# Kernel optimization log

Hardware: AMD Instinct MI355X
Metric: run time of the kernel (lower is better)

## Reference

```python
import jax, jax.numpy as jnp
import numpy as np

HID = 1024

def setup_inputs() -> dict:
    key = jax.random.key(0)
    k1, k2, k3, k4, k5 = jax.random.split(key, 5)
    B, S, H = 32, 2048, HID
    hidden = jax.random.normal(k1, (B, H), dtype=jnp.float32)
    encoder_outputs = jax.random.normal(k2, (B, S, 2 * H), dtype=jnp.float32)
    # nn.Linear(3H, H): weight (H, 3H), bias (H); nn.Linear(H, 1, bias=False): weight (1, H)
    lim_a = 1.0 / np.sqrt(3 * H)
    attn_w = jax.random.uniform(k3, (H, 3 * H), minval=-lim_a, maxval=lim_a, dtype=jnp.float32)
    attn_b = jax.random.uniform(k4, (H,), minval=-lim_a, maxval=lim_a, dtype=jnp.float32)
    lim_v = 1.0 / np.sqrt(H)
    v_w = jax.random.uniform(k5, (H,), minval=-lim_v, maxval=lim_v, dtype=jnp.float32)
    return {"hidden": hidden, "encoder_outputs": encoder_outputs,
            "attn_w": attn_w, "attn_b": attn_b, "v_w": v_w}

def reference(hidden, encoder_outputs, attn_w, attn_b, v_w):
    H = hidden.shape[-1]
    # Split attn weight: columns [:H] act on the repeated hidden, [H:] on encoder_outputs.
    # Avoids materializing the (B, S, 3H) concat; math is identical.
    w_h = attn_w[:, :H]        # (H, H)
    w_e = attn_w[:, H:]        # (H, 2H)
    hid_proj = hidden @ w_h.T + attn_b            # (B, H)
    enc_proj = jnp.einsum('bse,he->bsh', encoder_outputs, w_e)  # (B, S, H)
    energy = jnp.tanh(hid_proj[:, None, :] + enc_proj)          # (B, S, H)
    scores = jnp.einsum('bsh,h->bs', energy, v_w)               # (B, S)
    attention_weights = jax.nn.softmax(scores, axis=1)          # (B, S)
    context = jnp.einsum('bs,bse->be', attention_weights, encoder_outputs)  # (B, 2H)
    return (context, attention_weights)
```

## Files before the change

### kernel.cpp

```cpp
#include <hip/hip_runtime.h>
#include <hip/hip_bf16.h>

#define AS1 __attribute__((address_space(1)))
#define AS3 __attribute__((address_space(3)))

typedef __attribute__((ext_vector_type(4))) float  f32x4;
typedef __attribute__((ext_vector_type(8))) __bf16 bf16x8;
typedef __attribute__((ext_vector_type(2))) __bf16 bf16x2;
typedef __attribute__((ext_vector_type(4))) unsigned int uint4_;

static __device__ __forceinline__ unsigned short f2bf_rne(float f) {
    unsigned int u = __builtin_bit_cast(unsigned int, f);
    u += 0x7fffu + ((u >> 16) & 1u);
    return (unsigned short)(u >> 16);
}

static __device__ __forceinline__ unsigned int pack2(float a, float b) {
#if __has_builtin(__builtin_amdgcn_cvt_pk_bf16_f32)
    bf16x2 r = __builtin_amdgcn_cvt_pk_bf16_f32(a, b);
    return __builtin_bit_cast(unsigned int, r);
#else
    return (unsigned int)f2bf_rne(a) | ((unsigned int)f2bf_rne(b) << 16);
#endif
}

__global__ __launch_bounds__(256) void convwe_kernel(
    const float* __restrict__ attn_w, unsigned short* __restrict__ Bw)
{
    const int idx = (blockIdx.x * 256 + threadIdx.x) * 8;
    const int h = idx >> 11;
    const int e = idx & 2047;
    const float* src = attn_w + h * 3072 + 1024 + e;
    f32x4 v0 = *(const f32x4*)src;
    f32x4 v1 = *(const f32x4*)(src + 4);
    uint4_ o;
    o.x = pack2(v0.x, v0.y); o.y = pack2(v0.z, v0.w);
    o.z = pack2(v1.x, v1.y); o.w = pack2(v1.z, v1.w);
    *(uint4_*)(Bw + idx) = o;
}

__global__ __launch_bounds__(256) void convenc_kernel(
    const float* __restrict__ enc, unsigned short* __restrict__ dst)
{
    const size_t idx = ((size_t)blockIdx.x * 256 + threadIdx.x) * 8;
    f32x4 v0 = *(const f32x4*)(enc + idx);
    f32x4 v1 = *(const f32x4*)(enc + idx + 4);
    uint4_ o;
    o.x = pack2(v0.x, v0.y); o.y = pack2(v0.z, v0.w);
    o.z = pack2(v1.x, v1.y); o.w = pack2(v1.z, v1.w);
    *(uint4_*)(dst + idx) = o;
}

__global__ __launch_bounds__(256) void hidproj_kernel(
    const float* __restrict__ hidden, const float* __restrict__ attn_w,
    const float* __restrict__ attn_b, float* __restrict__ hp)
{
    __shared__ float wrow[1024];
    const int h = blockIdx.x;
    const int t = threadIdx.x;
#pragma unroll
    for (int i = 0; i < 4; ++i) wrow[t + i * 256] = attn_w[h * 3072 + t + i * 256];
    __syncthreads();
    const int wave = t >> 6, lane = t & 63;
    const float bias = attn_b[h];
    for (int b = wave; b < 32; b += 4) {
        float s = 0.f;
#pragma unroll
        for (int j = 0; j < 16; ++j)
            s = fmaf(hidden[b * 1024 + lane + j * 64], wrow[lane + j * 64], s);
#pragma unroll
        for (int off = 1; off < 64; off <<= 1) s += __shfl_xor(s, off);
        if (lane == 0) hp[b * 1024 + h] = s + bias;
    }
}

__global__ __launch_bounds__(256) void gemm_score_bf16_kernel(
    const unsigned short* __restrict__ Abf,
    const unsigned short* __restrict__ Bw,
    const float* __restrict__ hp,
    const float* __restrict__ vw,
    float* __restrict__ scores)
{
    __shared__ unsigned short As[128 * 32];
    __shared__ unsigned short Bs[128 * 32];

    const int id    = blockIdx.x;
    const int group = id >> 6;
    const int lid   = id & 63;
    const int mt    = group * 8 + (lid & 7);
    const int nt    = lid >> 3;
    const long tile_m = (long)mt * 128;
    const int  tile_n = nt * 128;

    const int t    = threadIdx.x;
    const int wave = t >> 6;
    const int lane = t & 63;
    const int quad = lane >> 4;
    const int l15  = lane & 15;

    const int ca = wave * 64 + lane;
    const int cb = (4 + wave) * 64 + lane;
    const unsigned short* apg0 = Abf + (tile_m + (ca >> 2)) * 2048 + (ca & 3) * 8;
    const unsigned short* apg1 = Abf + (tile_m + (cb >> 2)) * 2048 + (cb & 3) * 8;
    const unsigned short* bpg0 = Bw + (size_t)(tile_n + (ca >> 2)) * 2048 + (ca & 3) * 8;
    const unsigned short* bpg1 = Bw + (size_t)(tile_n + (cb >> 2)) * 2048 + (cb & 3) * 8;
    unsigned short* ald0 = &As[wave * 512];
    unsigned short* ald1 = &As[(4 + wave) * 512];
    unsigned short* bld0 = &Bs[wave * 512];
    unsigned short* bld1 = &Bs[(4 + wave) * 512];

    const int wm = (wave >> 1) * 64;
    const int wn = (wave & 1) * 64;

    int aoff[4], boff[4];
#pragma unroll
    for (int i = 0; i < 4; ++i) {
        aoff[i] = (wm + i * 16 + l15) * 32 + quad * 8;
        boff[i] = (wn + i * 16 + l15) * 32 + quad * 8;
    }

    f32x4 acc[4][4];
#pragma unroll
    for (int i = 0; i < 4; ++i)
#pragma unroll
        for (int j = 0; j < 4; ++j) acc[i][j] = (f32x4){0.f, 0.f, 0.f, 0.f};

    for (int kt = 0; kt < 64; ++kt) {
        __syncthreads();
        __builtin_amdgcn_global_load_lds((const AS1 void*)apg0, (AS3 void*)ald0, 16, 0, 0);
        __builtin_amdgcn_global_load_lds((const AS1 void*)apg1, (AS3 void*)ald1, 16, 0, 0);
        __builtin_amdgcn_global_load_lds((const AS1 void*)bpg0, (AS3 void*)bld0, 16, 0, 0);
        __builtin_amdgcn_global_load_lds((const AS1 void*)bpg1, (AS3 void*)bld1, 16, 0, 0);
        apg0 += 32; apg1 += 32; bpg0 += 32; bpg1 += 32;
        __syncthreads();

        bf16x8 af[4], bfr[4];
#pragma unroll
        for (int i = 0; i < 4; ++i) af[i]  = *(const bf16x8*)(&As[aoff[i]]);
#pragma unroll
        for (int i = 0; i < 4; ++i) bfr[i] = *(const bf16x8*)(&Bs[boff[i]]);
#pragma unroll
        for (int mi = 0; mi < 4; ++mi)
#pragma unroll
            for (int ni = 0; ni < 4; ++ni)
                acc[mi][ni] = __builtin_amdgcn_mfma_f32_16x16x32_bf16(
                    af[mi], bfr[ni], acc[mi][ni], 0, 0, 0);
    }

    const int bidx = mt >> 4;
    float vwv[4], hpv[4];
#pragma unroll
    for (int ni = 0; ni < 4; ++ni) {
        const int n = tile_n + wn + ni * 16 + l15;
        vwv[ni] = vw[n];
        hpv[ni] = hp[bidx * 1024 + n];
    }
#pragma unroll
    for (int mi = 0; mi < 4; ++mi) {
#pragma unroll
        for (int r = 0; r < 4; ++r) {
            float s = 0.f;
#pragma unroll
            for (int ni = 0; ni < 4; ++ni) {
                float x = hpv[ni] + acc[mi][ni][r];
                x = fminf(fmaxf(x, -12.f), 12.f);
                const float e  = __expf(x + x);
                const float th = (e - 1.f) * __builtin_amdgcn_rcpf(e + 1.f);
                s = fmaf(vwv[ni], th, s);
            }
            s += __shfl_xor(s, 1);
            s += __shfl_xor(s, 2);
            s += __shfl_xor(s, 4);
            s += __shfl_xor(s, 8);
            if (l15 == 0)
                atomicAdd(&scores[tile_m + wm + mi * 16 + quad * 4 + r], s);
        }
    }
}

__global__ __launch_bounds__(256) void gemm_score_kernel(
    const float* __restrict__ A, const unsigned short* __restrict__ Bw,
    const float* __restrict__ hp, const float* __restrict__ vw,
    float* __restrict__ scores)
{
    __shared__ unsigned short As[128 * 32];
    __shared__ unsigned short Bs[128 * 32];
    const int id    = blockIdx.x;
    const int group = id >> 6;
    const int lid   = id & 63;
    const int mt    = group * 8 + (lid & 7);
    const int nt    = lid >> 3;
    const long tile_m = (long)mt * 128;
    const int  tile_n = nt * 128;
    const int t = threadIdx.x, wave = t >> 6, lane = t & 63;
    const int quad = lane >> 4, l15 = lane & 15;
    const int arow = t >> 2, akc = (t & 3) * 8;
    const float* aptr0 = A + (tile_m + arow) * 2048 + akc;
    const float* aptr1 = aptr0 + 64 * 2048;
    unsigned short* ad0 = &As[t * 8];
    unsigned short* ad1 = &As[(256 + t) * 8];
    const int bc0 = wave * 128 + lane;
    const int bc1 = bc0 + 64;
    const unsigned short* bptr0 = Bw + (tile_n + (bc0 >> 2)) * 2048 + (bc0 & 3) * 8;
    const unsigned short* bptr1 = Bw + (tile_n + (bc1 >> 2)) * 2048 + (bc1 & 3) * 8;
    unsigned short* bd0 = &Bs[(wave * 2 + 0) * 512];
    unsigned short* bd1 = &Bs[(wave * 2 + 1) * 512];
    const int wm = (wave >> 1) * 64, wn = (wave & 1) * 64;
    int aoff[4], boff[4];
#pragma unroll
    for (int i = 0; i < 4; ++i) {
        aoff[i] = (wm + i * 16 + l15) * 32 + quad * 8;
        boff[i] = (wn + i * 16 + l15) * 32 + quad * 8;
    }
    f32x4 acc[4][4];
#pragma unroll
    for (int i = 0; i < 4; ++i)
#pragma unroll
        for (int j = 0; j < 4; ++j) acc[i][j] = (f32x4){0.f, 0.f, 0.f, 0.f};
    f32x4 av0 = *(const f32x4*)aptr0;
    f32x4 av1 = *(const f32x4*)(aptr0 + 4);
    f32x4 av2 = *(const f32x4*)aptr1;
    f32x4 av3 = *(const f32x4*)(aptr1 + 4);
    for (int kt = 0; kt < 64; ++kt) {
        __syncthreads();
        __builtin_amdgcn_global_load_lds((const AS1 void*)bptr0, (AS3 void*)bd0, 16, 0, 0);
        __builtin_amdgcn_global_load_lds((const AS1 void*)bptr1, (AS3 void*)bd1, 16, 0, 0);
        bptr0 += 32; bptr1 += 32;
        uint4_ w0, w1;
        w0.x = pack2(av0.x, av0.y); w0.y = pack2(av0.z, av0.w);
        w0.z = pack2(av1.x, av1.y); w0.w = pack2(av1.z, av1.w);
        w1.x = pack2(av2.x, av2.y); w1.y = pack2(av2.z, av2.w);
        w1.z = pack2(av3.x, av3.y); w1.w = pack2(av3.z, av3.w);
        *(uint4_*)ad0 = w0;
        *(uint4_*)ad1 = w1;
        if (kt < 63) {
            aptr0 += 32; aptr1 += 32;
            av0 = *(const f32x4*)aptr0;
            av1 = *(const f32x4*)(aptr0 + 4);
            av2 = *(const f32x4*)aptr1;
            av3 = *(const f32x4*)(aptr1 + 4);
        }
        __syncthreads();
        bf16x8 af[4], bfr[4];
#pragma unroll
        for (int i = 0; i < 4; ++i) af[i]  = *(const bf16x8*)(&As[aoff[i]]);
#pragma unroll
        for (int i = 0; i < 4; ++i) bfr[i] = *(const bf16x8*)(&Bs[boff[i]]);
#pragma unroll
        for (int mi = 0; mi < 4; ++mi)
#pragma unroll
            for (int ni = 0; ni < 4; ++ni)
                acc[mi][ni] = __builtin_amdgcn_mfma_f32_16x16x32_bf16(
                    af[mi], bfr[ni], acc[mi][ni], 0, 0, 0);
    }
    const int bidx = mt >> 4;
    float vwv[4], hpv[4];
#pragma unroll
    for (int ni = 0; ni < 4; ++ni) {
        const int n = tile_n + wn + ni * 16 + l15;
        vwv[ni] = vw[n];
        hpv[ni] = hp[bidx * 1024 + n];
    }
#pragma unroll
    for (int mi = 0; mi < 4; ++mi) {
#pragma unroll
        for (int r = 0; r < 4; ++r) {
            float s = 0.f;
#pragma unroll
            for (int ni = 0; ni < 4; ++ni) {
                float x = hpv[ni] + acc[mi][ni][r];
                x = fminf(fmaxf(x, -12.f), 12.f);
                const float e  = __expf(x + x);
                const float th = (e - 1.f) * __builtin_amdgcn_rcpf(e + 1.f);
                s = fmaf(vwv[ni], th, s);
            }
            s += __shfl_xor(s, 1);
            s += __shfl_xor(s, 2);
            s += __shfl_xor(s, 4);
            s += __shfl_xor(s, 8);
            if (l15 == 0)
                atomicAdd(&scores[tile_m + wm + mi * 16 + quad * 4 + r], s);
        }
    }
}

__global__ __launch_bounds__(256) void softmax_kernel(float* __restrict__ sc)
{
    __shared__ float red[8];
    const int b = blockIdx.x, t = threadIdx.x;
    const int wave = t >> 6, lane = t & 63;
    float* p = sc + b * 2048;
    float v[8];
#pragma unroll
    for (int i = 0; i < 8; ++i) v[i] = p[t + i * 256];
    float m = v[0];
#pragma unroll
    for (int i = 1; i < 8; ++i) m = fmaxf(m, v[i]);
#pragma unroll
    for (int off = 1; off < 64; off <<= 1) m = fmaxf(m, __shfl_xor(m, off));
    if (lane == 0) red[wave] = m;
    __syncthreads();
    m = fmaxf(fmaxf(red[0], red[1]), fmaxf(red[2], red[3]));
    float s = 0.f;
#pragma unroll
    for (int i = 0; i < 8; ++i) { v[i] = __expf(v[i] - m); s += v[i]; }
#pragma unroll
    for (int off = 1; off < 64; off <<= 1) s += __shfl_xor(s, off);
    if (lane == 0) red[4 + wave] = s;
    __syncthreads();
    s = red[4] + red[5] + red[6] + red[7];
    const float inv = 1.0f / s;
#pragma unroll
    for (int i = 0; i < 8; ++i) p[t + i * 256] = v[i] * inv;
}

__global__ __launch_bounds__(256) void context_part_kernel(
    const float* __restrict__ enc, const float* __restrict__ attn,
    float* __restrict__ part)
{
    const int b  = blockIdx.x >> 4;
    const int sc = blockIdx.x & 15;
    const int t  = threadIdx.x;
    const float* ep = enc + ((size_t)(b * 2048 + sc * 128)) * 2048 + t * 8;
    const float* ap = attn + b * 2048 + sc * 128;
    f32x4 a0 = (f32x4){0.f, 0.f, 0.f, 0.f};
    f32x4 a1 = (f32x4){0.f, 0.f, 0.f, 0.f};
#pragma unroll 4
    for (int s = 0; s < 128; ++s) {
        const float w = ap[s];
        f32x4 v0 = *(const f32x4*)ep;
        f32x4 v1 = *(const f32x4*)(ep + 4);
        a0 += w * v0;
        a1 += w * v1;
        ep += 2048;
    }
    float* pp = part + ((size_t)(b * 16 + sc)) * 2048 + t * 8;
    *(f32x4*)pp = a0;
    *(f32x4*)(pp + 4) = a1;
}

__global__ __launch_bounds__(256) void context_reduce_kernel(
    const float* __restrict__ part, float* __restrict__ ctx)
{
    const int idx = blockIdx.x * 256 + threadIdx.x;
    const int b = idx >> 11, e = idx & 2047;
    const float* pp = part + ((size_t)b * 16) * 2048 + e;
    float s = 0.f;
#pragma unroll
    for (int i = 0; i < 16; ++i) s += pp[i * 2048];
    ctx[idx] = s;
}

__global__ __launch_bounds__(256) void context_kernel(
    const float* __restrict__ enc, const float* __restrict__ attn,
    float* __restrict__ ctx)
{
    const int b  = blockIdx.x >> 5;
    const int sc = blockIdx.x & 31;
    const int t  = threadIdx.x;
    const float* ep = enc + ((long)(b * 2048 + sc * 64)) * 2048 + t * 8;
    const float* ap = attn + b * 2048 + sc * 64;
    f32x4 a0 = (f32x4){0.f, 0.f, 0.f, 0.f};
    f32x4 a1 = (f32x4){0.f, 0.f, 0.f, 0.f};
#pragma unroll 4
    for (int s = 0; s < 64; ++s) {
        const float w = ap[s];
        f32x4 v0 = *(const f32x4*)ep;
        f32x4 v1 = *(const f32x4*)(ep + 4);
        a0 += w * v0;
        a1 += w * v1;
        ep += 2048;
    }
    float* cp = ctx + b * 2048 + t * 8;
    atomicAdd(&cp[0], a0.x); atomicAdd(&cp[1], a0.y);
    atomicAdd(&cp[2], a0.z); atomicAdd(&cp[3], a0.w);
    atomicAdd(&cp[4], a1.x); atomicAdd(&cp[5], a1.y);
    atomicAdd(&cp[6], a1.z); atomicAdd(&cp[7], a1.w);
}

extern "C" void kernel_launch(void* const* d_in, const int* in_sizes, int n_in,
                              void* d_out, int out_size, void* d_ws, size_t ws_size,
                              hipStream_t stream)
{
    const float* hidden = (const float*)d_in[0];
    const float* enc    = (const float*)d_in[1];
    const float* attn_w = (const float*)d_in[2];
    const float* attn_b = (const float*)d_in[3];
    const float* vw     = (const float*)d_in[4];
    float* out = (float*)d_out;

    const size_t off_Bw   = 0;
    const size_t off_hp   = (size_t)1024 * 2048 * 2;
    const size_t off_part = off_hp + (size_t)32 * 1024 * 4;
    const size_t off_enc  = off_part + (size_t)512 * 2048 * 4;
    const size_t need_part = off_enc;
    const size_t need_full = off_enc + (size_t)65536 * 2048 * 2;

    unsigned short* Bw   = (unsigned short*)((char*)d_ws + off_Bw);
    float*          hp   = (float*)((char*)d_ws + off_hp);
    float*          part = (float*)((char*)d_ws + off_part);
    unsigned short* encbf= (unsigned short*)((char*)d_ws + off_enc);

    float* ctx  = out;
    float* attn = out + 65536;

    hipMemsetAsync(d_out, 0, (size_t)out_size * 4, stream);
    convwe_kernel <<<1024, 256, 0, stream>>>(attn_w, Bw);
    hidproj_kernel<<<1024, 256, 0, stream>>>(hidden, attn_w, attn_b, hp);

    if (ws_size >= need_full) {
        convenc_kernel<<<65536, 256, 0, stream>>>(enc, encbf);
        gemm_score_bf16_kernel<<<4096, 256, 0, stream>>>(encbf, Bw, hp, vw, attn);
    } else {
        gemm_score_kernel<<<4096, 256, 0, stream>>>(enc, Bw, hp, vw, attn);
    }

    softmax_kernel<<<32, 256, 0, stream>>>(attn);

    if (ws_size >= need_part) {
        context_part_kernel  <<<512, 256, 0, stream>>>(enc, attn, part);
        context_reduce_kernel<<<256, 256, 0, stream>>>(part, ctx);
    } else {
        context_kernel<<<1024, 256, 0, stream>>>(enc, attn, ctx);
    }
}
```

Baseline: 1.167 ms.

## Rewrite bf16 score GEMM as 256x256 multi-stage pipelined kernel

Replaces the 128x128 single-buffered bf16 GEMM with a 512-thread, 256x256-tile kernel. It uses a 4-slot LDS ring filled by direct global-to-LDS loads, XOR-swizzled LDS addressing, interleaved half-tile MFMA phases with s_setprio, and explicit vmcnt waits so loads overlap compute. Blocks are remapped with a swizzle for L2 reuse. The enc conversion kernel also becomes a grid-stride loop with far fewer blocks. The change aims to cut the per-k-step barrier stalls and raise reuse per loaded byte, at the cost of 128KB LDS per block and fragile hand-counted wait logic.

```diff
diff --git a/kernel.cpp b/kernel.cpp
--- a/kernel.cpp
+++ b/kernel.cpp
@@ -42,13 +42,18 @@
 __global__ __launch_bounds__(256) void convenc_kernel(
     const float* __restrict__ enc, unsigned short* __restrict__ dst)
 {
-    const size_t idx = ((size_t)blockIdx.x * 256 + threadIdx.x) * 8;
-    f32x4 v0 = *(const f32x4*)(enc + idx);
-    f32x4 v1 = *(const f32x4*)(enc + idx + 4);
-    uint4_ o;
-    o.x = pack2(v0.x, v0.y); o.y = pack2(v0.z, v0.w);
-    o.z = pack2(v1.x, v1.y); o.w = pack2(v1.z, v1.w);
-    *(uint4_*)(dst + idx) = o;
+    size_t idx = ((size_t)blockIdx.x * 256 + threadIdx.x) * 8;
+    const size_t step = (size_t)2048 * 256 * 8;
+#pragma unroll 4
+    for (int i = 0; i < 32; ++i) {
+        f32x4 v0 = *(const f32x4*)(enc + idx);
+        f32x4 v1 = *(const f32x4*)(enc + idx + 4);
+        uint4_ o;
+        o.x = pack2(v0.x, v0.y); o.y = pack2(v0.z, v0.w);
+        o.z = pack2(v1.x, v1.y); o.w = pack2(v1.z, v1.w);
+        *(uint4_*)(dst + idx) = o;
+        idx += step;
+    }
 }
 
 __global__ __launch_bounds__(256) void hidproj_kernel(
@@ -74,89 +79,144 @@
     }
 }
 
-__global__ __launch_bounds__(256) void gemm_score_bf16_kernel(
+__global__ __launch_bounds__(512, 2) void gemm8_score_kernel(
     const unsigned short* __restrict__ Abf,
     const unsigned short* __restrict__ Bw,
     const float* __restrict__ hp,
     const float* __restrict__ vw,
     float* __restrict__ scores)
 {
-    __shared__ unsigned short As[128 * 32];
-    __shared__ unsigned short Bs[128 * 32];
-
-    const int id    = blockIdx.x;
-    const int group = id >> 6;
-    const int lid   = id & 63;
-    const int mt    = group * 8 + (lid & 7);
-    const int nt    = lid >> 3;
-    const long tile_m = (long)mt * 128;
-    const int  tile_n = nt * 128;
-
-    const int t    = threadIdx.x;
-    const int wave = t >> 6;
-    const int lane = t & 63;
+    __shared__ unsigned short lds[65536];
+
+    const int bid = blockIdx.x;
+    const int swz = (bid & 7) * 128 + (bid >> 3);
+    const int mt  = swz >> 2;
+    const int nt  = swz & 3;
+    const long tile_m = (long)mt * 256;
+    const int  tile_n = nt * 256;
+
+    const int tid  = threadIdx.x;
+    const int w    = tid >> 6;
+    const int lane = tid & 63;
     const int quad = lane >> 4;
     const int l15  = lane & 15;
-
-    const int ca = wave * 64 + lane;
-    const int cb = (4 + wave) * 64 + lane;
-    const unsigned short* apg0 = Abf + (tile_m + (ca >> 2)) * 2048 + (ca & 3) * 8;
-    const unsigned short* apg1 = Abf + (tile_m + (cb >> 2)) * 2048 + (cb & 3) * 8;
-    const unsigned short* bpg0 = Bw + (size_t)(tile_n + (ca >> 2)) * 2048 + (ca & 3) * 8;
-    const unsigned short* bpg1 = Bw + (size_t)(tile_n + (cb >> 2)) * 2048 + (cb & 3) * 8;
-    unsigned short* ald0 = &As[wave * 512];
-    unsigned short* ald1 = &As[(4 + wave) * 512];
-    unsigned short* bld0 = &Bs[wave * 512];
-    unsigned short* bld1 = &Bs[(4 + wave) * 512];
-
-    const int wm = (wave >> 1) * 64;
-    const int wn = (wave & 1) * 64;
-
-    int aoff[4], boff[4];
-#pragma unroll
-    for (int i = 0; i < 4; ++i) {
-        aoff[i] = (wm + i * 16 + l15) * 32 + quad * 8;
-        boff[i] = (wn + i * 16 + l15) * 32 + quad * 8;
-    }
-
-    f32x4 acc[4][4];
-#pragma unroll
-    for (int i = 0; i < 4; ++i)
+    const int wm   = w >> 2;
+    const int wn   = w & 3;
+
+    const int wrow0 = (w * 2 + 0) * 16 + (lane >> 2);
+    const int wrow1 = (w * 2 + 1) * 16 + (lane >> 2);
+    const int wk8   = (lane & 3) ^ ((lane >> 3) & 3);
+    const unsigned short* aS0 = Abf + (size_t)(tile_m + wrow0) * 2048 + wk8 * 8;
+    const unsigned short* aS1 = Abf + (size_t)(tile_m + wrow1) * 2048 + wk8 * 8;
+    const unsigned short* bS0 = Bw  + (size_t)(tile_n + wrow0) * 2048 + wk8 * 8;
+    const unsigned short* bS1 = Bw  + (size_t)(tile_n + wrow1) * 2048 + wk8 * 8;
+    const int ld0 = (w * 2 + 0) * 512;
+    const int ld1 = (w * 2 + 1) * 512;
+
+    const int qsw   = (quad ^ ((l15 >> 1) & 3)) * 8;
+    const int aoffL = (wm * 128 + l15) * 32 + qsw;
+    const int boffL = 32768 + (wn * 64 + l15) * 32 + qsw;
+
+    f32x4 acc[8][4];
+#pragma unroll
+    for (int i = 0; i < 8; ++i)
 #pragma unroll
         for (int j = 0; j < 4; ++j) acc[i][j] = (f32x4){0.f, 0.f, 0.f, 0.f};
 
-    for (int kt = 0; kt < 64; ++kt) {
-        __syncthreads();
-        __builtin_amdgcn_global_load_lds((const AS1 void*)apg0, (AS3 void*)ald0, 16, 0, 0);
-        __builtin_amdgcn_global_load_lds((const AS1 void*)apg1, (AS3 void*)ald1, 16, 0, 0);
-        __builtin_amdgcn_global_load_lds((const AS1 void*)bpg0, (AS3 void*)bld0, 16, 0, 0);
-        __builtin_amdgcn_global_load_lds((const AS1 void*)bpg1, (AS3 void*)bld1, 16, 0, 0);
-        apg0 += 32; apg1 += 32; bpg0 += 32; bpg1 += 32;
-        __syncthreads();
-
-        bf16x8 af[4], bfr[4];
-#pragma unroll
-        for (int i = 0; i < 4; ++i) af[i]  = *(const bf16x8*)(&As[aoff[i]]);
-#pragma unroll
-        for (int i = 0; i < 4; ++i) bfr[i] = *(const bf16x8*)(&Bs[boff[i]]);
+#define G2L(srcp, dsti) __builtin_amdgcn_global_load_lds((const AS1 void*)(srcp), (AS3 void*)(&lds[(dsti)]), 16, 0, 0)
+#define ISSA(hs) do { const int sb_ = ((hs) & 3) * 8192;             \
+        G2L(aS0 + (size_t)(hs) * 32, sb_ + ld0);                     \
+        G2L(aS1 + (size_t)(hs) * 32, sb_ + ld1); } while (0)
+#define ISSB(hs) do { const int sb_ = 32768 + ((hs) & 3) * 8192;     \
+        G2L(bS0 + (size_t)(hs) * 32, sb_ + ld0);                     \
+        G2L(bS1 + (size_t)(hs) * 32, sb_ + ld1); } while (0)
+#define BARX() do { asm volatile("" ::: "memory"); __builtin_amdgcn_s_barrier(); asm volatile("" ::: "memory"); } while (0)
+
+    ISSA(0); ISSB(0); ISSA(1); ISSB(1); ISSA(2); ISSB(2);
+    asm volatile("s_waitcnt vmcnt(8)" ::: "memory");
+    BARX();
+
+    bf16x8 af[4], bfr[4];
+#pragma unroll 2
+    for (int kt = 0; kt < 32; ++kt) {
+        const int s0 = (2 * kt) & 3;
+        const int s1 = (2 * kt + 1) & 3;
+
+        if (kt < 31) ISSA(2 * kt + 3);
+#pragma unroll
+        for (int i = 0; i < 4; ++i) af[i]  = *(const bf16x8*)&lds[s0 * 8192 + aoffL + i * 512];
+#pragma unroll
+        for (int i = 0; i < 4; ++i) bfr[i] = *(const bf16x8*)&lds[s0 * 8192 + boffL + i * 512];
+        BARX();
+        __builtin_amdgcn_s_setprio(1);
 #pragma unroll
         for (int mi = 0; mi < 4; ++mi)
 #pragma unroll
             for (int ni = 0; ni < 4; ++ni)
-                acc[mi][ni] = __builtin_amdgcn_mfma_f32_16x16x32_bf16(
-                    af[mi], bfr[ni], acc[mi][ni], 0, 0, 0);
-    }
-
-    const int bidx = mt >> 4;
+                acc[mi][ni] = __builtin_amdgcn_mfma_f32_16x16x32_bf16(af[mi], bfr[ni], acc[mi][ni], 0, 0, 0);
+        __builtin_amdgcn_s_setprio(0);
+        BARX();
+
+        if (kt < 31) ISSB(2 * kt + 3);
+#pragma unroll
+        for (int i = 0; i < 4; ++i) af[i] = *(const bf16x8*)&lds[s0 * 8192 + aoffL + (4 + i) * 512];
+        BARX();
+        __builtin_amdgcn_s_setprio(1);
+#pragma unroll
+        for (int mi = 0; mi < 4; ++mi)
+#pragma unroll
+            for (int ni = 0; ni < 4; ++ni)
+                acc[4 + mi][ni] = __builtin_amdgcn_mfma_f32_16x16x32_bf16(af[mi], bfr[ni], acc[4 + mi][ni], 0, 0, 0);
+        __builtin_amdgcn_s_setprio(0);
+        if (kt < 31) { asm volatile("s_waitcnt vmcnt(8)" ::: "memory"); }
+        else         { asm volatile("s_waitcnt vmcnt(0)" ::: "memory"); }
+        BARX();
+
+        if (kt < 30) ISSA(2 * kt + 4);
+#pragma unroll
+        for (int i = 0; i < 4; ++i) af[i]  = *(const bf16x8*)&lds[s1 * 8192 + aoffL + i * 512];
+#pragma unroll
+        for (int i = 0; i < 4; ++i) bfr[i] = *(const bf16x8*)&lds[s1 * 8192 + boffL + i * 512];
+        BARX();
+        __builtin_amdgcn_s_setprio(1);
+#pragma unroll
+        for (int mi = 0; mi < 4; ++mi)
+#pragma unroll
+            for (int ni = 0; ni < 4; ++ni)
+                acc[mi][ni] = __builtin_amdgcn_mfma_f32_16x16x32_bf16(af[mi], bfr[ni], acc[mi][ni], 0, 0, 0);
+        __builtin_amdgcn_s_setprio(0);
+        BARX();
+
+        if (kt < 30) ISSB(2 * kt + 4);
+#pragma unroll
+        for (int i = 0; i < 4; ++i) af[i] = *(const bf16x8*)&lds[s1 * 8192 + aoffL + (4 + i) * 512];
+        BARX();
+        __builtin_amdgcn_s_setprio(1);
+#pragma unroll
+        for (int mi = 0; mi < 4; ++mi)
+#pragma unroll
+            for (int ni = 0; ni < 4; ++ni)
+                acc[4 + mi][ni] = __builtin_amdgcn_mfma_f32_16x16x32_bf16(af[mi], bfr[ni], acc[4 + mi][ni], 0, 0, 0);
+        __builtin_amdgcn_s_setprio(0);
+        if (kt < 30) { asm volatile("s_waitcnt vmcnt(8)" ::: "memory"); }
+        else         { asm volatile("s_waitcnt vmcnt(4)" ::: "memory"); }
+        BARX();
+    }
+#undef G2L
+#undef ISSA
+#undef ISSB
+#undef BARX
+
+    const int bidx = (int)(tile_m >> 11);
     float vwv[4], hpv[4];
 #pragma unroll
     for (int ni = 0; ni < 4; ++ni) {
-        const int n = tile_n + wn + ni * 16 + l15;
+        const int n = tile_n + wn * 64 + ni * 16 + l15;
         vwv[ni] = vw[n];
         hpv[ni] = hp[bidx * 1024 + n];
     }
 #pragma unroll
-    for (int mi = 0; mi < 4; ++mi) {
+    for (int mi = 0; mi < 8; ++mi) {
 #pragma unroll
         for (int r = 0; r < 4; ++r) {
             float s = 0.f;
@@ -173,7 +233,7 @@
             s += __shfl_xor(s, 4);
             s += __shfl_xor(s, 8);
             if (l15 == 0)
-                atomicAdd(&scores[tile_m + wm + mi * 16 + quad * 4 + r], s);
+                atomicAdd(&scores[tile_m + wm * 128 + mi * 16 + quad * 4 + r], s);
         }
     }
 }
@@ -409,8 +469,8 @@
     hidproj_kernel<<<1024, 256, 0, stream>>>(hidden, attn_w, attn_b, hp);
 
     if (ws_size >= need_full) {
-        convenc_kernel<<<65536, 256, 0, stream>>>(enc, encbf);
-        gemm_score_bf16_kernel<<<4096, 256, 0, stream>>>(encbf, Bw, hp, vw, attn);
+        convenc_kernel<<<2048, 256, 0, stream>>>(enc, encbf);
+        gemm8_score_kernel<<<1024, 512, 0, stream>>>(encbf, Bw, hp, vw, attn);
     } else {
         gemm_score_kernel<<<4096, 256, 0, stream>>>(enc, Bw, hp, vw, attn);
     }
```

Result: faster. 1.125 ms (-3.6%).

## Fuse fp32-to-bf16 conversion into a 256x256 double-buffered score GEMM

Applied to the files above, without the earlier changes.

Drops the separate pass that converted the whole encoder tensor to bf16. A new 512-thread kernel with 256x256 tiles loads fp32 A into registers, converts it and writes it to swizzled LDS. It double-buffers the A and B tiles, staggers barriers and raises wave priority around the MFMA blocks, which removes a large extra read/write of the activations and overlaps loads with compute. The context partial reduction is also split into 64-row chunks for more blocks. The trade-off is higher register and LDS pressure, about 128KB of LDS per block, and more complex hand-scheduled waitcnt logic.

```diff
diff --git a/kernel.cpp b/kernel.cpp
--- a/kernel.cpp
+++ b/kernel.cpp
@@ -39,18 +39,6 @@
     *(uint4_*)(Bw + idx) = o;
 }
 
-__global__ __launch_bounds__(256) void convenc_kernel(
-    const float* __restrict__ enc, unsigned short* __restrict__ dst)
-{
-    const size_t idx = ((size_t)blockIdx.x * 256 + threadIdx.x) * 8;
-    f32x4 v0 = *(const f32x4*)(enc + idx);
-    f32x4 v1 = *(const f32x4*)(enc + idx + 4);
-    uint4_ o;
-    o.x = pack2(v0.x, v0.y); o.y = pack2(v0.z, v0.w);
-    o.z = pack2(v1.x, v1.y); o.w = pack2(v1.z, v1.w);
-    *(uint4_*)(dst + idx) = o;
-}
-
 __global__ __launch_bounds__(256) void hidproj_kernel(
     const float* __restrict__ hidden, const float* __restrict__ attn_w,
     const float* __restrict__ attn_b, float* __restrict__ hp)
@@ -74,89 +62,182 @@
     }
 }
 
-__global__ __launch_bounds__(256) void gemm_score_bf16_kernel(
-    const unsigned short* __restrict__ Abf,
+__global__ __launch_bounds__(512, 2) void gemm8f_score_kernel(
+    const float* __restrict__ enc,
     const unsigned short* __restrict__ Bw,
     const float* __restrict__ hp,
     const float* __restrict__ vw,
     float* __restrict__ scores)
 {
-    __shared__ unsigned short As[128 * 32];
-    __shared__ unsigned short Bs[128 * 32];
-
-    const int id    = blockIdx.x;
-    const int group = id >> 6;
-    const int lid   = id & 63;
-    const int mt    = group * 8 + (lid & 7);
-    const int nt    = lid >> 3;
-    const long tile_m = (long)mt * 128;
-    const int  tile_n = nt * 128;
-
-    const int t    = threadIdx.x;
-    const int wave = t >> 6;
-    const int lane = t & 63;
+    __shared__ unsigned short lds[65536];
+
+    const int bid = blockIdx.x;
+    const int swz = (bid & 7) * 128 + (bid >> 3);
+    const int mt  = swz >> 2;
+    const int nt  = swz & 3;
+    const long tile_m = (long)mt * 256;
+    const int  tile_n = nt * 256;
+
+    const int tid  = threadIdx.x;
+    const int w    = tid >> 6;
+    const int lane = tid & 63;
     const int quad = lane >> 4;
     const int l15  = lane & 15;
-
-    const int ca = wave * 64 + lane;
-    const int cb = (4 + wave) * 64 + lane;
-    const unsigned short* apg0 = Abf + (tile_m + (ca >> 2)) * 2048 + (ca & 3) * 8;
-    const unsigned short* apg1 = Abf + (tile_m + (cb >> 2)) * 2048 + (cb & 3) * 8;
-    const unsigned short* bpg0 = Bw + (size_t)(tile_n + (ca >> 2)) * 2048 + (ca & 3) * 8;
-    const unsigned short* bpg1 = Bw + (size_t)(tile_n + (cb >> 2)) * 2048 + (cb & 3) * 8;
-    unsigned short* ald0 = &As[wave * 512];
-    unsigned short* ald1 = &As[(4 + wave) * 512];
-    unsigned short* bld0 = &Bs[wave * 512];
-    unsigned short* bld1 = &Bs[(4 + wave) * 512];
-
-    const int wm = (wave >> 1) * 64;
-    const int wn = (wave & 1) * 64;
-
-    int aoff[4], boff[4];
-#pragma unroll
-    for (int i = 0; i < 4; ++i) {
-        aoff[i] = (wm + i * 16 + l15) * 32 + quad * 8;
-        boff[i] = (wn + i * 16 + l15) * 32 + quad * 8;
-    }
-
-    f32x4 acc[4][4];
-#pragma unroll
-    for (int i = 0; i < 4; ++i)
+    const int wm   = w >> 2;
+    const int wn   = w & 3;
+
+    const int arow = tid >> 1;
+    const int ah4  = (tid & 1) * 4;
+    const int ar7  = arow & 7;
+    const float* ap = enc + (size_t)(tile_m + arow) * 2048 + (tid & 1) * 32;
+    const int awb  = arow * 64;
+    const int awo0 = awb + ((ah4 + 0) ^ ar7) * 8;
+    const int awo1 = awb + ((ah4 + 1) ^ ar7) * 8;
+    const int awo2 = awb + ((ah4 + 2) ^ ar7) * 8;
+    const int awo3 = awb + ((ah4 + 3) ^ ar7) * 8;
+
+    const int brl = lane >> 3;
+    const int bk8 = (lane & 7) ^ brl;
+    const unsigned short* bp = Bw + (size_t)(tile_n + w * 32 + brl) * 2048 + bk8 * 8;
+
+    const int l7  = l15 & 7;
+    const int arb = (wm * 128 + l15) * 64;
+    const int brb = (wn * 64 + l15) * 64;
+    const int sw0 = ((quad)     ^ l7) * 8;
+    const int sw1 = ((quad + 4) ^ l7) * 8;
+
+    f32x4 acc[8][4];
+#pragma unroll
+    for (int i = 0; i < 8; ++i)
 #pragma unroll
         for (int j = 0; j < 4; ++j) acc[i][j] = (f32x4){0.f, 0.f, 0.f, 0.f};
 
-    for (int kt = 0; kt < 64; ++kt) {
-        __syncthreads();
-        __builtin_amdgcn_global_load_lds((const AS1 void*)apg0, (AS3 void*)ald0, 16, 0, 0);
-        __builtin_amdgcn_global_load_lds((const AS1 void*)apg1, (AS3 void*)ald1, 16, 0, 0);
-        __builtin_amdgcn_global_load_lds((const AS1 void*)bpg0, (AS3 void*)bld0, 16, 0, 0);
-        __builtin_amdgcn_global_load_lds((const AS1 void*)bpg1, (AS3 void*)bld1, 16, 0, 0);
-        apg0 += 32; apg1 += 32; bpg0 += 32; bpg1 += 32;
-        __syncthreads();
-
-        bf16x8 af[4], bfr[4];
-#pragma unroll
-        for (int i = 0; i < 4; ++i) af[i]  = *(const bf16x8*)(&As[aoff[i]]);
-#pragma unroll
-        for (int i = 0; i < 4; ++i) bfr[i] = *(const bf16x8*)(&Bs[boff[i]]);
-#pragma unroll
-        for (int mi = 0; mi < 4; ++mi)
-#pragma unroll
-            for (int ni = 0; ni < 4; ++ni)
-                acc[mi][ni] = __builtin_amdgcn_mfma_f32_16x16x32_bf16(
-                    af[mi], bfr[ni], acc[mi][ni], 0, 0, 0);
-    }
-
-    const int bidx = mt >> 4;
+    f32x4 av0, av1, av2, av3, av4, av5, av6, av7;
+    bf16x8 af[4], bfr[4];
+    int ak = 0, kb = 0;
+
+#define G2L(srcp, dsti) __builtin_amdgcn_global_load_lds((const AS1 void*)(srcp), (AS3 void*)(&lds[(dsti)]), 16, 0, 0)
+#define PRIO1 __builtin_amdgcn_s_setprio(1)
+#define PRIO0 __builtin_amdgcn_s_setprio(0)
+#define BARX() do { asm volatile("" ::: "memory"); __builtin_amdgcn_s_barrier(); asm volatile("" ::: "memory"); } while (0)
+
+#define ISSB(NXT) do {                                              \
+    const unsigned short* bs_ = bp + kb;                            \
+    const int bd_ = 32768 + (NXT) * 16384 + w * 2048;               \
+    G2L(bs_,          bd_);                                         \
+    G2L(bs_ + 16384,  bd_ + 512);                                   \
+    G2L(bs_ + 32768,  bd_ + 1024);                                  \
+    G2L(bs_ + 49152,  bd_ + 1536);                                  \
+} while (0)
+
+#define LOADA() do {                                                \
+    const float* as_ = ap + ak;                                     \
+    av0 = *(const f32x4*)(as_);      av1 = *(const f32x4*)(as_ + 4);  \
+    av2 = *(const f32x4*)(as_ + 8);  av3 = *(const f32x4*)(as_ + 12); \
+    av4 = *(const f32x4*)(as_ + 16); av5 = *(const f32x4*)(as_ + 20); \
+    av6 = *(const f32x4*)(as_ + 24); av7 = *(const f32x4*)(as_ + 28); \
+} while (0)
+
+#define CONVA(NXT) do {                                             \
+    const int ab_ = (NXT) * 16384;                                  \
+    uint4_ q_;                                                      \
+    q_.x = pack2(av0.x, av0.y); q_.y = pack2(av0.z, av0.w);         \
+    q_.z = pack2(av1.x, av1.y); q_.w = pack2(av1.z, av1.w);         \
+    *(uint4_*)&lds[ab_ + awo0] = q_;                                \
+    q_.x = pack2(av2.x, av2.y); q_.y = pack2(av2.z, av2.w);         \
+    q_.z = pack2(av3.x, av3.y); q_.w = pack2(av3.z, av3.w);         \
+    *(uint4_*)&lds[ab_ + awo1] = q_;                                \
+    q_.x = pack2(av4.x, av4.y); q_.y = pack2(av4.z, av4.w);         \
+    q_.z = pack2(av5.x, av5.y); q_.w = pack2(av5.z, av5.w);         \
+    *(uint4_*)&lds[ab_ + awo2] = q_;                                \
+    q_.x = pack2(av6.x, av6.y); q_.y = pack2(av6.z, av6.w);         \
+    q_.z = pack2(av7.x, av7.y); q_.w = pack2(av7.z, av7.w);         \
+    *(uint4_*)&lds[ab_ + awo3] = q_;                                \
+} while (0)
+
+#define RDA(CUR, MB, SW) do {                                       \
+    const int aa_ = (CUR) * 16384 + arb + (SW);                     \
+    af[0] = *(const bf16x8*)&lds[aa_ + ((MB) + 0) * 1024];          \
+    af[1] = *(const bf16x8*)&lds[aa_ + ((MB) + 1) * 1024];          \
+    af[2] = *(const bf16x8*)&lds[aa_ + ((MB) + 2) * 1024];          \
+    af[3] = *(const bf16x8*)&lds[aa_ + ((MB) + 3) * 1024];          \
+} while (0)
+
+#define RDB(CUR, SW) do {                                           \
+    const int bb_ = 32768 + (CUR) * 16384 + brb + (SW);             \
+    bfr[0] = *(const bf16x8*)&lds[bb_];                             \
+    bfr[1] = *(const bf16x8*)&lds[bb_ + 1024];                      \
+    bfr[2] = *(const bf16x8*)&lds[bb_ + 2048];                      \
+    bfr[3] = *(const bf16x8*)&lds[bb_ + 3072];                      \
+} while (0)
+
+#define MFMA_BLK(MB) do {                                           \
+    _Pragma("unroll")                                               \
+    for (int mi = 0; mi < 4; ++mi)                                  \
+    _Pragma("unroll")                                               \
+        for (int ni = 0; ni < 4; ++ni)                              \
+            acc[(MB) + mi][ni] = __builtin_amdgcn_mfma_f32_16x16x32_bf16( \
+                af[mi], bfr[ni], acc[(MB) + mi][ni], 0, 0, 0);      \
+} while (0)
+
+#define TILE(CUR, NXT, DO_B, DO_CONV, DO_NA, EW, DO_END) do {       \
+                                                            \
+    if (DO_B) { ISSB(NXT); kb += 64; }                              \
+    RDA(CUR, 0, sw0); RDB(CUR, sw0);                                \
+    BARX(); PRIO1; MFMA_BLK(0); PRIO0; BARX();                      \
+                                                            \
+    RDA(CUR, 4, sw0);                                               \
+    BARX(); PRIO1; MFMA_BLK(4); PRIO0; BARX();                      \
+                                                            \
+    RDA(CUR, 0, sw1); RDB(CUR, sw1);                                \
+    BARX(); PRIO1; MFMA_BLK(0); PRIO0; BARX();                      \
+                                                            \
+    RDA(CUR, 4, sw1);                                               \
+    if (DO_CONV) CONVA(NXT);                                        \
+    if (DO_NA) { LOADA(); ak += 64; }                               \
+    BARX(); PRIO1; MFMA_BLK(4); PRIO0;                              \
+    if (DO_END) {                                                   \
+        asm volatile("s_waitcnt " EW " lgkmcnt(0)" ::: "memory");   \
+        BARX();                                                     \
+    }                                                               \
+} while (0)
+
+    LOADA(); ak += 64;
+    ISSB(0); kb += 64;
+    CONVA(0);
+    LOADA(); ak += 64;
+    asm volatile("s_waitcnt vmcnt(8) lgkmcnt(0)" ::: "memory");
+    BARX();
+
+    for (int kt = 0; kt < 30; kt += 2) {
+        TILE(0, 1, 1, 1, 1, "vmcnt(8)", 1);
+        TILE(1, 0, 1, 1, 1, "vmcnt(8)", 1);
+    }
+    TILE(0, 1, 1, 1, 0, "vmcnt(0)", 1);
+    TILE(1, 0, 0, 0, 0, "", 0);
+
+#undef G2L
+#undef PRIO1
+#undef PRIO0
+#undef BARX
+#undef ISSB
+#undef LOADA
+#undef CONVA
+#undef RDA
+#undef RDB
+#undef MFMA_BLK
+#undef TILE
+
+    const int bidx = (int)(tile_m >> 11);
     float vwv[4], hpv[4];
 #pragma unroll
     for (int ni = 0; ni < 4; ++ni) {
-        const int n = tile_n + wn + ni * 16 + l15;
+        const int n = tile_n + wn * 64 + ni * 16 + l15;
         vwv[ni] = vw[n];
         hpv[ni] = hp[bidx * 1024 + n];
     }
 #pragma unroll
-    for (int mi = 0; mi < 4; ++mi) {
+    for (int mi = 0; mi < 8; ++mi) {
 #pragma unroll
         for (int r = 0; r < 4; ++r) {
             float s = 0.f;
@@ -173,113 +254,7 @@
             s += __shfl_xor(s, 4);
             s += __shfl_xor(s, 8);
             if (l15 == 0)
-                atomicAdd(&scores[tile_m + wm + mi * 16 + quad * 4 + r], s);
-        }
-    }
-}
-
-__global__ __launch_bounds__(256) void gemm_score_kernel(
-    const float* __restrict__ A, const unsigned short* __restrict__ Bw,
-    const float* __restrict__ hp, const float* __restrict__ vw,
-    float* __restrict__ scores)
-{
-    __shared__ unsigned short As[128 * 32];
-    __shared__ unsigned short Bs[128 * 32];
-    const int id    = blockIdx.x;
-    const int group = id >> 6;
-    const int lid   = id & 63;
-    const int mt    = group * 8 + (lid & 7);
-    const int nt    = lid >> 3;
-    const long tile_m = (long)mt * 128;
-    const int  tile_n = nt * 128;
-    const int t = threadIdx.x, wave = t >> 6, lane = t & 63;
-    const int quad = lane >> 4, l15 = lane & 15;
-    const int arow = t >> 2, akc = (t & 3) * 8;
-    const float* aptr0 = A + (tile_m + arow) * 2048 + akc;
-    const float* aptr1 = aptr0 + 64 * 2048;
-    unsigned short* ad0 = &As[t * 8];
-    unsigned short* ad1 = &As[(256 + t) * 8];
-    const int bc0 = wave * 128 + lane;
-    const int bc1 = bc0 + 64;
-    const unsigned short* bptr0 = Bw + (tile_n + (bc0 >> 2)) * 2048 + (bc0 & 3) * 8;
-    const unsigned short* bptr1 = Bw + (tile_n + (bc1 >> 2)) * 2048 + (bc1 & 3) * 8;
-    unsigned short* bd0 = &Bs[(wave * 2 + 0) * 512];
-    unsigned short* bd1 = &Bs[(wave * 2 + 1) * 512];
-    const int wm = (wave >> 1) * 64, wn = (wave & 1) * 64;
-    int aoff[4], boff[4];
-#pragma unroll
-    for (int i = 0; i < 4; ++i) {
-        aoff[i] = (wm + i * 16 + l15) * 32 + quad * 8;
-        boff[i] = (wn + i * 16 + l15) * 32 + quad * 8;
-    }
-    f32x4 acc[4][4];
-#pragma unroll
-    for (int i = 0; i < 4; ++i)
-#pragma unroll
-        for (int j = 0; j < 4; ++j) acc[i][j] = (f32x4){0.f, 0.f, 0.f, 0.f};
-    f32x4 av0 = *(const f32x4*)aptr0;
-    f32x4 av1 = *(const f32x4*)(aptr0 + 4);
-    f32x4 av2 = *(const f32x4*)aptr1;
-    f32x4 av3 = *(const f32x4*)(aptr1 + 4);
-    for (int kt = 0; kt < 64; ++kt) {
-        __syncthreads();
-        __builtin_amdgcn_global_load_lds((const AS1 void*)bptr0, (AS3 void*)bd0, 16, 0, 0);
-        __builtin_amdgcn_global_load_lds((const AS1 void*)bptr1, (AS3 void*)bd1, 16, 0, 0);
-        bptr0 += 32; bptr1 += 32;
-        uint4_ w0, w1;
-        w0.x = pack2(av0.x, av0.y); w0.y = pack2(av0.z, av0.w);
-        w0.z = pack2(av1.x, av1.y); w0.w = pack2(av1.z, av1.w);
-        w1.x = pack2(av2.x, av2.y); w1.y = pack2(av2.z, av2.w);
-        w1.z = pack2(av3.x, av3.y); w1.w = pack2(av3.z, av3.w);
-        *(uint4_*)ad0 = w0;
-        *(uint4_*)ad1 = w1;
-        if (kt < 63) {
-            aptr0 += 32; aptr1 += 32;
-            av0 = *(const f32x4*)aptr0;
-            av1 = *(const f32x4*)(aptr0 + 4);
-            av2 = *(const f32x4*)aptr1;
-            av3 = *(const f32x4*)(aptr1 + 4);
-        }
-        __syncthreads();
-        bf16x8 af[4], bfr[4];
-#pragma unroll
-        for (int i = 0; i < 4; ++i) af[i]  = *(const bf16x8*)(&As[aoff[i]]);
-#pragma unroll
-        for (int i = 0; i < 4; ++i) bfr[i] = *(const bf16x8*)(&Bs[boff[i]]);
-#pragma unroll
-        for (int mi = 0; mi < 4; ++mi)
-#pragma unroll
-            for (int ni = 0; ni < 4; ++ni)
-                acc[mi][ni] = __builtin_amdgcn_mfma_f32_16x16x32_bf16(
-                    af[mi], bfr[ni], acc[mi][ni], 0, 0, 0);
-    }
-    const int bidx = mt >> 4;
-    float vwv[4], hpv[4];
-#pragma unroll
-    for (int ni = 0; ni < 4; ++ni) {
-        const int n = tile_n + wn + ni * 16 + l15;
-        vwv[ni] = vw[n];
-        hpv[ni] = hp[bidx * 1024 + n];
-    }
-#pragma unroll
-    for (int mi = 0; mi < 4; ++mi) {
-#pragma unroll
-        for (int r = 0; r < 4; ++r) {
-            float s = 0.f;
-#pragma unroll
-            for (int ni = 0; ni < 4; ++ni) {
-                float x = hpv[ni] + acc[mi][ni][r];
-                x = fminf(fmaxf(x, -12.f), 12.f);
-                const float e  = __expf(x + x);
-                const float th = (e - 1.f) * __builtin_amdgcn_rcpf(e + 1.f);
-                s = fmaf(vwv[ni], th, s);
-            }
-            s += __shfl_xor(s, 1);
-            s += __shfl_xor(s, 2);
-            s += __shfl_xor(s, 4);
-            s += __shfl_xor(s, 8);
-            if (l15 == 0)
-                atomicAdd(&scores[tile_m + wm + mi * 16 + quad * 4 + r], s);
+                atomicAdd(&scores[tile_m + wm * 128 + mi * 16 + quad * 4 + r], s);
         }
     }
 }
@@ -318,15 +293,15 @@
     const float* __restrict__ enc, const float* __restrict__ attn,
     float* __restrict__ part)
 {
-    const int b  = blockIdx.x >> 4;
-    const int sc = blockIdx.x & 15;
+    const int b  = blockIdx.x >> 5;
+    const int sc = blockIdx.x & 31;
     const int t  = threadIdx.x;
-    const float* ep = enc + ((size_t)(b * 2048 + sc * 128)) * 2048 + t * 8;
-    const float* ap = attn + b * 2048 + sc * 128;
+    const float* ep = enc + ((size_t)(b * 2048 + sc * 64)) * 2048 + t * 8;
+    const float* ap = attn + b * 2048 + sc * 64;
     f32x4 a0 = (f32x4){0.f, 0.f, 0.f, 0.f};
     f32x4 a1 = (f32x4){0.f, 0.f, 0.f, 0.f};
 #pragma unroll 4
-    for (int s = 0; s < 128; ++s) {
+    for (int s = 0; s < 64; ++s) {
         const float w = ap[s];
         f32x4 v0 = *(const f32x4*)ep;
         f32x4 v1 = *(const f32x4*)(ep + 4);
@@ -334,7 +309,7 @@
         a1 += w * v1;
         ep += 2048;
     }
-    float* pp = part + ((size_t)(b * 16 + sc)) * 2048 + t * 8;
+    float* pp = part + ((size_t)(b * 32 + sc)) * 2048 + t * 8;
     *(f32x4*)pp = a0;
     *(f32x4*)(pp + 4) = a1;
 }
@@ -344,10 +319,10 @@
 {
     const int idx = blockIdx.x * 256 + threadIdx.x;
     const int b = idx >> 11, e = idx & 2047;
-    const float* pp = part + ((size_t)b * 16) * 2048 + e;
+    const float* pp = part + ((size_t)b * 32) * 2048 + e;
     float s = 0.f;
 #pragma unroll
-    for (int i = 0; i < 16; ++i) s += pp[i * 2048];
+    for (int i = 0; i < 32; ++i) s += pp[i * 2048];
     ctx[idx] = s;
 }
 
@@ -392,14 +367,11 @@
     const size_t off_Bw   = 0;
     const size_t off_hp   = (size_t)1024 * 2048 * 2;
     const size_t off_part = off_hp + (size_t)32 * 1024 * 4;
-    const size_t off_enc  = off_part + (size_t)512 * 2048 * 4;
-    const size_t need_part = off_enc;
-    const size_t need_full = off_enc + (size_t)65536 * 2048 * 2;
+    const size_t need_part = off_part + (size_t)1024 * 2048 * 4;
 
     unsigned short* Bw   = (unsigned short*)((char*)d_ws + off_Bw);
     float*          hp   = (float*)((char*)d_ws + off_hp);
     float*          part = (float*)((char*)d_ws + off_part);
-    unsigned short* encbf= (unsigned short*)((char*)d_ws + off_enc);
 
     float* ctx  = out;
     float* attn = out + 65536;
@@ -408,17 +380,12 @@
     convwe_kernel <<<1024, 256, 0, stream>>>(attn_w, Bw);
     hidproj_kernel<<<1024, 256, 0, stream>>>(hidden, attn_w, attn_b, hp);
 
-    if (ws_size >= need_full) {
-        convenc_kernel<<<65536, 256, 0, stream>>>(enc, encbf);
-        gemm_score_bf16_kernel<<<4096, 256, 0, stream>>>(encbf, Bw, hp, vw, attn);
-    } else {
-        gemm_score_kernel<<<4096, 256, 0, stream>>>(enc, Bw, hp, vw, attn);
-    }
+    gemm8f_score_kernel<<<1024, 512, 0, stream>>>(enc, Bw, hp, vw, attn);
 
     softmax_kernel<<<32, 256, 0, stream>>>(attn);
 
     if (ws_size >= need_part) {
-        context_part_kernel  <<<512, 256, 0, stream>>>(enc, attn, part);
+        context_part_kernel  <<<1024, 256, 0, stream>>>(enc, attn, part);
         context_reduce_kernel<<<256, 256, 0, stream>>>(part, ctx);
     } else {
         context_kernel<<<1024, 256, 0, stream>>>(enc, attn, ctx);
```

Result: slower. 1.236 ms (+5.9%).
